# Optimization experiments

Measured on AMD Instinct MI355X. Metric: run time of the kernel, lower is better.

## Reference

```python
import jax, jax.numpy as jnp
import numpy as np
import math

# SOMI config constants (SOMIBrainConfig defaults assumed)
ALPHA_1 = 1.0      # Laplacian coupling strength
ALPHA_0 = 0.1      # local restoring term
DT = 0.1           # integration step
TARGET_ZETA = 1.0  # damping ratio target
SPARSITY = 0.9     # fraction of W entries masked to zero

OMEGA_MED = math.sqrt(max(1e-08, ALPHA_1 * 1.0 + ALPHA_0 + 1.0))
BETA = 2.0 * TARGET_ZETA * OMEGA_MED
N_STEPS = max(3, min(10, int(math.pi / (OMEGA_MED * DT))))  # = 10

B, S, D = 4, 4096, 512


def setup_inputs() -> dict:
    key = jax.random.key(0)
    k1, k2, k3 = jax.random.split(key, 3)
    hidden_states = jax.random.normal(k1, (B, S, D), dtype=jnp.float32)
    # sparse interaction matrix W: ~(1-SPARSITY) fraction nonzero
    mask = (jax.random.uniform(k2, (D, D)) > SPARSITY).astype(jnp.float32)
    W = jax.random.normal(k3, (D, D), dtype=jnp.float32) * (1.0 / math.sqrt(D)) * mask
    gate_alpha = jnp.ones((1,), dtype=jnp.float32)  # nonzero so settling path runs
    precision = jnp.ones((D,), dtype=jnp.float32)   # 1/clamp(error_variance=1, 0.1)
    return {"hidden_states": hidden_states, "W": W, "gate_alpha": gate_alpha,
            "precision": precision}


def compute_laplacian(W):
    # random-walk Laplacian over hidden-dim graph: L_rw = I - D^{-1} A, A = |W|
    A = jnp.abs(W)
    deg = jnp.clip(A.sum(axis=-1), 1e-8, None)
    return jnp.eye(W.shape[0], dtype=W.dtype) - A / deg[:, None]


def settle(phi0, phi_target, L_rw, precision, beta, n_steps):
    # damped second-order SOMI field equation on the hidden dim,
    # semi-implicit Euler integration, n_steps fixed steps
    def step(carry, _):
        phi, phi_dot = carry
        # Laplacian acting on the hidden dimension: (L_rw @ phi^T)^T
        coupling = jnp.einsum('bsd,ed->bse', phi, L_rw)
        force = (-ALPHA_1 * coupling - ALPHA_0 * phi
                 + precision * (phi_target - phi) - beta * phi_dot)
        phi_dot = phi_dot + DT * force
        phi = phi + DT * phi_dot
        return (phi, phi_dot), None
    (phi, phi_dot), _ = jax.lax.scan(step, (phi0, jnp.zeros_like(phi0)),
                                     None, length=n_steps)
    return phi, phi_dot


def reference(hidden_states, W, gate_alpha, precision):
    gate = jnp.tanh(gate_alpha)[0]
    L_rw = compute_laplacian(W)
    phi_settled, _ = settle(hidden_states, hidden_states, L_rw, precision,
                            BETA, N_STEPS)
    return hidden_states + gate * (phi_settled - hidden_states)
```

## Files before the change

### kernel.cpp

```cpp
#include <hip/hip_runtime.h>
#include <stdint.h>

#define D_DIM 512
#define NSTEPS 10
#define ALPHA0 0.1
#define DT_C 0.1
#define BETA_C 2.8982753492378875

typedef __attribute__((ext_vector_type(8))) short short8;
typedef __attribute__((ext_vector_type(4))) float floatx4;

__device__ __forceinline__ unsigned short f32_to_bf16(float f) {
    union { float f; uint32_t u; } v;
    v.f = f;
    uint32_t u = v.u;
    return (unsigned short)((u + 0x7FFFu + ((u >> 16) & 1u)) >> 16);
}
__device__ __forceinline__ float bf16_to_f32(unsigned short h) {
    union { uint32_t u; float f; } v;
    v.u = ((uint32_t)h) << 16;
    return v.f;
}
__device__ __forceinline__ short8 pack8(const float4 v0, const float4 v1) {
    short8 pk;
    pk[0] = (short)f32_to_bf16(v0.x); pk[1] = (short)f32_to_bf16(v0.y);
    pk[2] = (short)f32_to_bf16(v0.z); pk[3] = (short)f32_to_bf16(v0.w);
    pk[4] = (short)f32_to_bf16(v1.x); pk[5] = (short)f32_to_bf16(v1.y);
    pk[6] = (short)f32_to_bf16(v1.z); pk[7] = (short)f32_to_bf16(v1.w);
    return pk;
}

__device__ __forceinline__ size_t aform_off(int r, int k) {
    return ((size_t)((r >> 5) * 32 + (k >> 5) * 2 + ((r >> 4) & 1)) << 10)
         + (size_t)(((((k >> 3) & 3) * 16) + (r & 15)) << 4) + (size_t)((k & 7) * 2);
}
__device__ __forceinline__ size_t gtl_off(int e, int c) {
    return ((size_t)((e >> 4) * 16 + (c >> 5)) << 10)
         + (size_t)(((((c >> 3) & 3) * 16) + (e & 15)) << 4) + (size_t)((c & 7) * 2);
}

__global__ __launch_bounds__(64) void prep2(
    const float* __restrict__ W,
    const float* __restrict__ prec,
    unsigned short* __restrict__ AfM,
    unsigned short* __restrict__ BfM)
{
    const int e = blockIdx.x;
    const int lane = threadIdx.x;
    const float* w = W + (size_t)e * D_DIM + lane * 8;
    const float4 v0 = *(const float4*)w;
    const float4 v1 = *(const float4*)(w + 4);
    float a[8] = { fabsf(v0.x), fabsf(v0.y), fabsf(v0.z), fabsf(v0.w),
                   fabsf(v1.x), fabsf(v1.y), fabsf(v1.z), fabsf(v1.w) };
    float s = a[0] + a[1] + a[2] + a[3] + a[4] + a[5] + a[6] + a[7];
#pragma unroll
    for (int off = 1; off < 64; off <<= 1) s += __shfl_xor(s, off, 64);
    const float inv = 1.0f / fmaxf(s, 1e-8f);
    const float madd = (float)ALPHA0 + prec[e];
    unsigned short mv[8];
#pragma unroll
    for (int j = 0; j < 8; ++j) {
        const int d = lane * 8 + j;
        float lv = ((d == e) ? 1.0f : 0.0f) - a[j] * inv;
        if (d == e) lv += madd;
        mv[j] = f32_to_bf16(lv);
    }
    short8 pk;
#pragma unroll
    for (int j = 0; j < 8; ++j) pk[j] = (short)mv[j];
    *(short8*)((char*)AfM + aform_off(e, lane * 8)) = pk;
#pragma unroll
    for (int j = 0; j < 8; ++j) {
        const int d = lane * 8 + j;
        *(unsigned short*)((char*)BfM + aform_off(d, e)) = mv[j];
    }
}

template<int MODE>
__global__ __launch_bounds__(256) void pk(
    const unsigned short* __restrict__ Aop,
    const unsigned short* __restrict__ Bop,
    unsigned short* __restrict__ outA,
    unsigned short* __restrict__ outB,
    const unsigned short* __restrict__ BfM,
    const unsigned short* __restrict__ BfM2,
    const float* __restrict__ prec,
    const float* __restrict__ gate_alpha,
    float ca0, float cb0, float ca1, float cb1, float ca2, float cb2)
{
    const int tid = threadIdx.x;
    const int wave = tid >> 6, lane = tid & 63;
    const int lrow = lane & 15, q = lane >> 4;
    const int br = blockIdx.x >> 3, bc = blockIdx.x & 7;
    const int wr = wave >> 1, wc = wave & 1;
    const int rgA = br * 2 + wr;
    const int cgB = bc * 2 + wc;

    const char* abase = (const char*)Aop + ((size_t)(rgA * 32) << 10) + (size_t)lane * 16;
    const char* bbase = (const char*)Bop + ((size_t)(cgB * 32) << 10) + (size_t)lane * 16;

    floatx4 acc[2][2] = {};
#pragma unroll 4
    for (int kk = 0; kk < 16; ++kk) {
        short8 av0 = *(const short8*)(abase + ((kk * 2 + 0) << 10));
        short8 av1 = *(const short8*)(abase + ((kk * 2 + 1) << 10));
        short8 bv0 = *(const short8*)(bbase + ((kk * 2 + 0) << 10));
        short8 bv1 = *(const short8*)(bbase + ((kk * 2 + 1) << 10));
        acc[0][0] = __builtin_amdgcn_mfma_f32_16x16x32_bf16(av0, bv0, acc[0][0], 0, 0, 0);
        acc[0][1] = __builtin_amdgcn_mfma_f32_16x16x32_bf16(av0, bv1, acc[0][1], 0, 0, 0);
        acc[1][0] = __builtin_amdgcn_mfma_f32_16x16x32_bf16(av1, bv0, acc[1][0], 0, 0, 0);
        acc[1][1] = __builtin_amdgcn_mfma_f32_16x16x32_bf16(av1, bv1, acc[1][1], 0, 0, 0);
    }

    float g = 0.f;
    if (MODE == 3) g = tanhf(gate_alpha[0]);

#pragma unroll
    for (int n = 0; n < 2; ++n) {
        const int c = cgB * 32 + n * 16 + lrow;
        float g0 = 0.f, g1 = 0.f, g2 = 0.f;
        if (MODE >= 2) {
            const float p = prec[c];
            g0 = ca0 + cb0 * p; g1 = ca1 + cb1 * p; g2 = ca2 + cb2 * p;
        }
#pragma unroll
        for (int m = 0; m < 2; ++m) {
            const int eb = rgA * 32 + m * 16;
#pragma unroll
            for (int j = 0; j < 4; ++j) {
                const int e = eb + q * 4 + j;
                float val = acc[m][n][j];
                if (MODE >= 2) {
                    const float Mec  = bf16_to_f32(*(const unsigned short*)((const char*)BfM  + aform_off(c, e)));
                    const float M2ec = bf16_to_f32(*(const unsigned short*)((const char*)BfM2 + aform_off(c, e)));
                    if (MODE == 2) {
                        val += g1 * Mec + g2 * M2ec;
                        if (e == c) val += g0;
                    } else {
                        val = g * (val + g1 * Mec + g2 * M2ec);
                        if (e == c) val += (1.0f - g) + g * g0;
                    }
                }
                const unsigned short h = f32_to_bf16(val);
                if (MODE == 0 || MODE == 1)
                    *(unsigned short*)((char*)outA + aform_off(e, c)) = h;
                if (MODE == 0 || MODE == 2)
                    *(unsigned short*)((char*)outB + aform_off(c, e)) = h;
                if (MODE == 3)
                    *(unsigned short*)((char*)outA + gtl_off(e, c)) = h;
            }
        }
    }
}

__global__ __launch_bounds__(256) void ek(
    const unsigned short* __restrict__ BfM,
    const unsigned short* __restrict__ BfM2,
    const float* __restrict__ prec,
    unsigned short* __restrict__ BfB2,
    float ca6, float cb6, float ca7, float cb7, float ca8, float cb8)
{
    const int chunk = blockIdx.x * 256 + threadIdx.x;
    const int half = chunk >> 6, l = chunk & 63;
    const int cg = half >> 5, rem = half & 31, kt = rem >> 1, h = rem & 1;
    const int c = cg * 32 + h * 16 + (l & 15);
    const int dbase = kt * 32 + (l >> 4) * 8;
    const float p = prec[c];
    const float g6 = ca6 + cb6 * p, g7 = ca7 + cb7 * p, g8 = ca8 + cb8 * p;
    const short8 vm  = ((const short8*)BfM)[chunk];
    const short8 vm2 = ((const short8*)BfM2)[chunk];
    short8 o;
#pragma unroll
    for (int u = 0; u < 8; ++u) {
        float v = g7 * bf16_to_f32((unsigned short)vm[u])
                + g8 * bf16_to_f32((unsigned short)vm2[u]);
        if (dbase + u == c) v += g6;
        o[u] = (short)f32_to_bf16(v);
    }
    ((short8*)BfB2)[chunk] = o;
}

__global__ __launch_bounds__(512, 2) void out_gemm(
    const float* __restrict__ H,
    const unsigned short* __restrict__ Gtl,
    float* __restrict__ Out)
{
    const int cpx = gridDim.x >> 3;
    const int bid = (blockIdx.x & 7) * cpx + (blockIdx.x >> 3);
    const int r0 = bid * 64;
    const int tid = threadIdx.x;
    const int wave = tid >> 6, lane = tid & 63;
    const int lrow = lane & 15, q = lane >> 4;

    __shared__ unsigned short hlds[64 * D_DIM];
    char* lds = (char*)hlds;

#pragma unroll
    for (int i = 0; i < 8; ++i) {
        const int row = wave * 8 + i;
        const float* src = H + (size_t)(r0 + row) * D_DIM + lane * 8;
        const float4 v0 = *(const float4*)src;
        const float4 v1 = *(const float4*)(src + 4);
        int byte = row * 1024 + lane * 16;
        byte ^= (row & 7) << 4;
        *(short8*)(lds + byte) = pack8(v0, v1);
    }
    __syncthreads();

    const char* gtb = (const char*)Gtl + ((size_t)(wave * 4 * 16) << 10)
                      + ((size_t)lane << 4);

    floatx4 acc[4][4] = {};
#pragma unroll 2
    for (int kk = 0; kk < 16; ++kk) {
        short8 b[4];
#pragma unroll
        for (int n = 0; n < 4; ++n)
            b[n] = *(const short8*)(gtb + ((size_t)(n * 16 + kk) << 10));
#pragma unroll
        for (int m = 0; m < 4; ++m) {
            const int row = m * 16 + lrow;
            int byte = row * 1024 + kk * 64 + q * 16;
            byte ^= (row & 7) << 4;
            const short8 a = *(const short8*)(lds + byte);
#pragma unroll
            for (int n = 0; n < 4; ++n)
                acc[m][n] = __builtin_amdgcn_mfma_f32_16x16x32_bf16(a, b[n], acc[m][n], 0, 0, 0);
        }
    }

#pragma unroll
    for (int m = 0; m < 4; ++m) {
#pragma unroll
        for (int j = 0; j < 4; ++j) {
            const int r = r0 + m * 16 + q * 4 + j;
#pragma unroll
            for (int n = 0; n < 4; ++n) {
                const int e = wave * 64 + n * 16 + lrow;
                Out[(size_t)r * D_DIM + e] = acc[m][n][j];
            }
        }
    }
}

extern "C" void kernel_launch(void* const* d_in, const int* in_sizes, int n_in,
                              void* d_out, int out_size, void* d_ws, size_t ws_size,
                              hipStream_t stream)
{
    const float* H    = (const float*)d_in[0];
    const float* W    = (const float*)d_in[1];
    const float* gate = (const float*)d_in[2];
    const float* prec = (const float*)d_in[3];
    float* out = (float*)d_out;
    char* ws = (char*)d_ws;

    double Pc[11] = {0}, Qc[11] = {0}, Rc[11] = {0}, Sc[11] = {0};
    Pc[0] = 1.0;
    const double dtd = DT_C, c1 = 1.0 - BETA_C * DT_C;
    for (int s = 0; s < NSTEPS; ++s) {
        double nR[11], nS[11];
        for (int k = 0; k < 11; ++k) {
            nR[k] = c1 * Rc[k] - dtd * (k > 0 ? Pc[k - 1] : 0.0);
            nS[k] = c1 * Sc[k] - dtd * (k > 0 ? Qc[k - 1] : 0.0);
        }
        nS[0] += dtd;
        for (int k = 0; k < 11; ++k) {
            Rc[k] = nR[k]; Sc[k] = nS[k];
            Pc[k] += dtd * nR[k]; Qc[k] += dtd * nS[k];
        }
    }
    float av[9], bv[9];
    for (int k = 0; k < 9; ++k) { av[k] = (float)Pc[k]; bv[k] = (float)Qc[k]; }

    unsigned short* AfM  = (unsigned short*)(ws);
    unsigned short* BfM  = (unsigned short*)(ws + (512u << 10));
    unsigned short* AfM2 = (unsigned short*)(ws + (1024u << 10));
    unsigned short* BfM2 = (unsigned short*)(ws + (1536u << 10));
    unsigned short* AfM3 = (unsigned short*)(ws + (2048u << 10));
    unsigned short* BfB2 = (unsigned short*)(ws + (2560u << 10));
    unsigned short* BfV  = (unsigned short*)(ws + (3072u << 10));
    unsigned short* Gtl  = (unsigned short*)(ws + (3584u << 10));

    prep2<<<dim3(D_DIM), dim3(64), 0, stream>>>(W, prec, AfM, BfM);

    pk<0><<<dim3(64), dim3(256), 0, stream>>>(
        AfM, BfM, AfM2, BfM2, nullptr, nullptr, nullptr, nullptr,
        0.f, 0.f, 0.f, 0.f, 0.f, 0.f);
    pk<1><<<dim3(64), dim3(256), 0, stream>>>(
        AfM2, BfM, AfM3, nullptr, nullptr, nullptr, nullptr, nullptr,
        0.f, 0.f, 0.f, 0.f, 0.f, 0.f);
    ek<<<dim3(128), dim3(256), 0, stream>>>(
        BfM, BfM2, prec, BfB2, av[6], bv[6], av[7], bv[7], av[8], bv[8]);
    pk<2><<<dim3(64), dim3(256), 0, stream>>>(
        AfM3, BfB2, nullptr, BfV, BfM, BfM2, prec, nullptr,
        av[3], bv[3], av[4], bv[4], av[5], bv[5]);
    pk<3><<<dim3(64), dim3(256), 0, stream>>>(
        AfM3, BfV, Gtl, nullptr, BfM, BfM2, prec, gate,
        av[0], bv[0], av[1], bv[1], av[2], bv[2]);

    out_gemm<<<dim3(16384 / 64), dim3(512), 0, stream>>>(H, Gtl, out);
}
```

Baseline: 58.92 us.

## Fuse ek into pk<2>, split pk into single-wave blocks, halve out_gemm row tile

Drops the separate ek elementwise kernel and computes the combined B operand (g6*I + g7*M + g8*M2) on the fly inside pk<2>'s K loop. It also switches the pk kernels from 4-wave blocks over 64 workgroups to single-wave blocks over 256 workgroups, spreading the small 512x512 polynomial GEMMs across more CUs. out_gemm now takes 32 rows per block instead of 64, doubling its grid to 512 blocks and halving LDS per block. The costs are lower per-block B-tile reuse in out_gemm, since each Gtl fragment now feeds half as many MFMAs, and redundant conversion work in pk<2>.

```diff
diff --git a/kernel.cpp b/kernel.cpp
--- a/kernel.cpp
+++ b/kernel.cpp
@@ -77,7 +77,7 @@
 }
 
 template<int MODE>
-__global__ __launch_bounds__(256) void pk(
+__global__ __launch_bounds__(64) void pk(
     const unsigned short* __restrict__ Aop,
     const unsigned short* __restrict__ Bop,
     unsigned short* __restrict__ outA,
@@ -86,26 +86,56 @@
     const unsigned short* __restrict__ BfM2,
     const float* __restrict__ prec,
     const float* __restrict__ gate_alpha,
-    float ca0, float cb0, float ca1, float cb1, float ca2, float cb2)
+    float ca0, float cb0, float ca1, float cb1, float ca2, float cb2,
+    float ca3, float cb3, float ca4, float cb4, float ca5, float cb5)
 {
-    const int tid = threadIdx.x;
-    const int wave = tid >> 6, lane = tid & 63;
+    const int lane = threadIdx.x;
     const int lrow = lane & 15, q = lane >> 4;
-    const int br = blockIdx.x >> 3, bc = blockIdx.x & 7;
-    const int wr = wave >> 1, wc = wave & 1;
-    const int rgA = br * 2 + wr;
-    const int cgB = bc * 2 + wc;
-
-    const char* abase = (const char*)Aop + ((size_t)(rgA * 32) << 10) + (size_t)lane * 16;
-    const char* bbase = (const char*)Bop + ((size_t)(cgB * 32) << 10) + (size_t)lane * 16;
+    const int rg = blockIdx.x >> 4;
+    const int cg = blockIdx.x & 15;
+
+    const char* abase = (const char*)Aop + ((size_t)(rg * 32) << 10) + (size_t)lane * 16;
+    const char* bbase = (const char*)Bop + ((size_t)(cg * 32) << 10) + (size_t)lane * 16;
+    const char* b2base = (const char*)BfM2 + ((size_t)(cg * 32) << 10) + (size_t)lane * 16;
+
+    float g6h[2], g7h[2], g8h[2];
+    int ch[2];
+    if (MODE == 2) {
+#pragma unroll
+        for (int h = 0; h < 2; ++h) {
+            ch[h] = cg * 32 + h * 16 + lrow;
+            const float p = prec[ch[h]];
+            g6h[h] = ca3 + cb3 * p; g7h[h] = ca4 + cb4 * p; g8h[h] = ca5 + cb5 * p;
+        }
+    }
 
     floatx4 acc[2][2] = {};
 #pragma unroll 4
     for (int kk = 0; kk < 16; ++kk) {
-        short8 av0 = *(const short8*)(abase + ((kk * 2 + 0) << 10));
-        short8 av1 = *(const short8*)(abase + ((kk * 2 + 1) << 10));
-        short8 bv0 = *(const short8*)(bbase + ((kk * 2 + 0) << 10));
-        short8 bv1 = *(const short8*)(bbase + ((kk * 2 + 1) << 10));
+        const short8 av0 = *(const short8*)(abase + ((kk * 2 + 0) << 10));
+        const short8 av1 = *(const short8*)(abase + ((kk * 2 + 1) << 10));
+        short8 bv0, bv1;
+        if (MODE == 2) {
+            const short8 m0 = *(const short8*)(bbase  + ((kk * 2 + 0) << 10));
+            const short8 m1 = *(const short8*)(bbase  + ((kk * 2 + 1) << 10));
+            const short8 n0 = *(const short8*)(b2base + ((kk * 2 + 0) << 10));
+            const short8 n1 = *(const short8*)(b2base + ((kk * 2 + 1) << 10));
+#pragma unroll
+            for (int u = 0; u < 8; ++u) {
+                const int k = kk * 32 + q * 8 + u;
+                float v0 = g7h[0] * bf16_to_f32((unsigned short)m0[u])
+                         + g8h[0] * bf16_to_f32((unsigned short)n0[u]);
+                if (k == ch[0]) v0 += g6h[0];
+                float v1 = g7h[1] * bf16_to_f32((unsigned short)m1[u])
+                         + g8h[1] * bf16_to_f32((unsigned short)n1[u]);
+                if (k == ch[1]) v1 += g6h[1];
+                bv0[u] = (short)f32_to_bf16(v0);
+                bv1[u] = (short)f32_to_bf16(v1);
+            }
+        } else {
+            bv0 = *(const short8*)(bbase + ((kk * 2 + 0) << 10));
+            bv1 = *(const short8*)(bbase + ((kk * 2 + 1) << 10));
+        }
         acc[0][0] = __builtin_amdgcn_mfma_f32_16x16x32_bf16(av0, bv0, acc[0][0], 0, 0, 0);
         acc[0][1] = __builtin_amdgcn_mfma_f32_16x16x32_bf16(av0, bv1, acc[0][1], 0, 0, 0);
         acc[1][0] = __builtin_amdgcn_mfma_f32_16x16x32_bf16(av1, bv0, acc[1][0], 0, 0, 0);
@@ -117,7 +147,7 @@
 
 #pragma unroll
     for (int n = 0; n < 2; ++n) {
-        const int c = cgB * 32 + n * 16 + lrow;
+        const int c = cg * 32 + n * 16 + lrow;
         float g0 = 0.f, g1 = 0.f, g2 = 0.f;
         if (MODE >= 2) {
             const float p = prec[c];
@@ -125,7 +155,7 @@
         }
 #pragma unroll
         for (int m = 0; m < 2; ++m) {
-            const int eb = rgA * 32 + m * 16;
+            const int eb = rg * 32 + m * 16;
 #pragma unroll
             for (int j = 0; j < 4; ++j) {
                 const int e = eb + q * 4 + j;
@@ -153,33 +183,6 @@
     }
 }
 
-__global__ __launch_bounds__(256) void ek(
-    const unsigned short* __restrict__ BfM,
-    const unsigned short* __restrict__ BfM2,
-    const float* __restrict__ prec,
-    unsigned short* __restrict__ BfB2,
-    float ca6, float cb6, float ca7, float cb7, float ca8, float cb8)
-{
-    const int chunk = blockIdx.x * 256 + threadIdx.x;
-    const int half = chunk >> 6, l = chunk & 63;
-    const int cg = half >> 5, rem = half & 31, kt = rem >> 1, h = rem & 1;
-    const int c = cg * 32 + h * 16 + (l & 15);
-    const int dbase = kt * 32 + (l >> 4) * 8;
-    const float p = prec[c];
-    const float g6 = ca6 + cb6 * p, g7 = ca7 + cb7 * p, g8 = ca8 + cb8 * p;
-    const short8 vm  = ((const short8*)BfM)[chunk];
-    const short8 vm2 = ((const short8*)BfM2)[chunk];
-    short8 o;
-#pragma unroll
-    for (int u = 0; u < 8; ++u) {
-        float v = g7 * bf16_to_f32((unsigned short)vm[u])
-                + g8 * bf16_to_f32((unsigned short)vm2[u]);
-        if (dbase + u == c) v += g6;
-        o[u] = (short)f32_to_bf16(v);
-    }
-    ((short8*)BfB2)[chunk] = o;
-}
-
 __global__ __launch_bounds__(512, 2) void out_gemm(
     const float* __restrict__ H,
     const unsigned short* __restrict__ Gtl,
@@ -187,17 +190,17 @@
 {
     const int cpx = gridDim.x >> 3;
     const int bid = (blockIdx.x & 7) * cpx + (blockIdx.x >> 3);
-    const int r0 = bid * 64;
+    const int r0 = bid * 32;
     const int tid = threadIdx.x;
     const int wave = tid >> 6, lane = tid & 63;
     const int lrow = lane & 15, q = lane >> 4;
 
-    __shared__ unsigned short hlds[64 * D_DIM];
+    __shared__ unsigned short hlds[32 * D_DIM];
     char* lds = (char*)hlds;
 
 #pragma unroll
-    for (int i = 0; i < 8; ++i) {
-        const int row = wave * 8 + i;
+    for (int i = 0; i < 4; ++i) {
+        const int row = wave * 4 + i;
         const float* src = H + (size_t)(r0 + row) * D_DIM + lane * 8;
         const float4 v0 = *(const float4*)src;
         const float4 v1 = *(const float4*)(src + 4);
@@ -210,7 +213,7 @@
     const char* gtb = (const char*)Gtl + ((size_t)(wave * 4 * 16) << 10)
                       + ((size_t)lane << 4);
 
-    floatx4 acc[4][4] = {};
+    floatx4 acc[2][4] = {};
 #pragma unroll 2
     for (int kk = 0; kk < 16; ++kk) {
         short8 b[4];
@@ -218,7 +221,7 @@
         for (int n = 0; n < 4; ++n)
             b[n] = *(const short8*)(gtb + ((size_t)(n * 16 + kk) << 10));
 #pragma unroll
-        for (int m = 0; m < 4; ++m) {
+        for (int m = 0; m < 2; ++m) {
             const int row = m * 16 + lrow;
             int byte = row * 1024 + kk * 64 + q * 16;
             byte ^= (row & 7) << 4;
@@ -230,7 +233,7 @@
     }
 
 #pragma unroll
-    for (int m = 0; m < 4; ++m) {
+    for (int m = 0; m < 2; ++m) {
 #pragma unroll
         for (int j = 0; j < 4; ++j) {
             const int r = r0 + m * 16 + q * 4 + j;
@@ -277,26 +280,25 @@
     unsigned short* AfM2 = (unsigned short*)(ws + (1024u << 10));
     unsigned short* BfM2 = (unsigned short*)(ws + (1536u << 10));
     unsigned short* AfM3 = (unsigned short*)(ws + (2048u << 10));
-    unsigned short* BfB2 = (unsigned short*)(ws + (2560u << 10));
-    unsigned short* BfV  = (unsigned short*)(ws + (3072u << 10));
-    unsigned short* Gtl  = (unsigned short*)(ws + (3584u << 10));
+    unsigned short* BfV  = (unsigned short*)(ws + (2560u << 10));
+    unsigned short* Gtl  = (unsigned short*)(ws + (3072u << 10));
 
     prep2<<<dim3(D_DIM), dim3(64), 0, stream>>>(W, prec, AfM, BfM);
 
-    pk<0><<<dim3(64), dim3(256), 0, stream>>>(
+    pk<0><<<dim3(256), dim3(64), 0, stream>>>(
         AfM, BfM, AfM2, BfM2, nullptr, nullptr, nullptr, nullptr,
+        0.f, 0.f, 0.f, 0.f, 0.f, 0.f, 0.f, 0.f, 0.f, 0.f, 0.f, 0.f);
+    pk<1><<<dim3(256), dim3(64), 0, stream>>>(
+        AfM2, BfM, AfM3, nullptr, nullptr, nullptr, nullptr, nullptr,
+        0.f, 0.f, 0.f, 0.f, 0.f, 0.f, 0.f, 0.f, 0.f, 0.f, 0.f, 0.f);
+    pk<2><<<dim3(256), dim3(64), 0, stream>>>(
+        AfM3, BfM, nullptr, BfV, BfM, BfM2, prec, nullptr,
+        av[3], bv[3], av[4], bv[4], av[5], bv[5],
+        av[6], bv[6], av[7], bv[7], av[8], bv[8]);
+    pk<3><<<dim3(256), dim3(64), 0, stream>>>(
+        AfM3, BfV, Gtl, nullptr, BfM, BfM2, prec, gate,
+        av[0], bv[0], av[1], bv[1], av[2], bv[2],
         0.f, 0.f, 0.f, 0.f, 0.f, 0.f);
-    pk<1><<<dim3(64), dim3(256), 0, stream>>>(
-        AfM2, BfM, AfM3, nullptr, nullptr, nullptr, nullptr, nullptr,
-        0.f, 0.f, 0.f, 0.f, 0.f, 0.f);
-    ek<<<dim3(128), dim3(256), 0, stream>>>(
-        BfM, BfM2, prec, BfB2, av[6], bv[6], av[7], bv[7], av[8], bv[8]);
-    pk<2><<<dim3(64), dim3(256), 0, stream>>>(
-        AfM3, BfB2, nullptr, BfV, BfM, BfM2, prec, nullptr,
-        av[3], bv[3], av[4], bv[4], av[5], bv[5]);
-    pk<3><<<dim3(64), dim3(256), 0, stream>>>(
-        AfM3, BfV, Gtl, nullptr, BfM, BfM2, prec, gate,
-        av[0], bv[0], av[1], bv[1], av[2], bv[2]);
-
-    out_gemm<<<dim3(16384 / 64), dim3(512), 0, stream>>>(H, Gtl, out);
-}
+
+    out_gemm<<<dim3(16384 / 32), dim3(512), 0, stream>>>(H, Gtl, out);
+}
```

Result: slower. 61.68 us (+4.7%).
